# Performance work log

Hardware: AMD Instinct MI355X
Metric: run time of the kernel (lower is better)

Reference implementation:

```python
import jax, jax.numpy as jnp
import numpy as np


def setup_inputs() -> dict:
    key = jax.random.key(0)
    k1, k2, k3, k4 = jax.random.split(key, 4)
    N, T, F = 8192, 128, 9
    M_s = 256
    merged = jax.random.normal(k1, (N, T, F), dtype=jnp.float32)
    input1 = jax.random.normal(k2, (N, T, F), dtype=jnp.float32)
    samples = jax.random.normal(k3, (N, M_s), dtype=jnp.float32)
    labels = jax.random.randint(k4, (N,), 0, 10, dtype=jnp.int32)
    return {"merged": merged, "input1": input1, "samples": samples, "labels": labels}


def reference(merged, input1, samples, labels):
    # Pairwise squared distances S_ij = sum_k (s_i - s_j)^2 / M_s, computed via
    # the Gram-matrix identity instead of materializing the [N, N, M_s] tensor.
    M_s = samples.shape[1]
    sq = jnp.sum(samples * samples, axis=-1)                 # [N]
    gram = jnp.einsum('im,jm->ij', samples, samples)         # [N, N]
    S_ij = (sq[:, None] + sq[None, :] - 2.0 * gram) / jnp.float32(M_s)
    same = (labels[:, None] == labels[None, :]).astype(jnp.float32)
    term2 = jnp.mean(jnp.maximum(0.0, (1.0 - same) * (1.0 - S_ij)))
    L_label = 10.0 * jnp.mean(same * S_ij) + 10.0 * term2
    return L_label
```

## Files before the change

kernel.cpp:

```cpp
#include <hip/hip_runtime.h>

#define NROWS 8192
#define KDIM  256
#define NT    64
#define NBLK  (NT * (NT + 1) / 2)
#define GRID  256

typedef __attribute__((ext_vector_type(4)))  float f32x4;
typedef __attribute__((ext_vector_type(16))) float f32x16;
typedef __attribute__((ext_vector_type(4)))  int   i32x4;
typedef __attribute__((ext_vector_type(8)))  int   i32x8;

#define GLD(gp, lp)                                                            \
  __builtin_amdgcn_global_load_lds(                                            \
      (const __attribute__((address_space(1))) void*)(gp),                     \
      (__attribute__((address_space(3))) void*)(lp), 16, 0, 0)

__global__ void prep_kernel(const float* __restrict__ samples,
                            const int* __restrict__ labels,
                            unsigned char* __restrict__ sf8,
                            float2* __restrict__ meta,
                            float* __restrict__ out) {
  int row = blockIdx.x, t = threadIdx.x;
  float2 v2 = ((const float2*)samples)[(size_t)row * 128 + t];
  int pk = __builtin_amdgcn_cvt_pk_fp8_f32(v2.x, v2.y, 0, false);
  ((unsigned short*)sf8)[(size_t)row * 128 + t] = (unsigned short)(pk & 0xffff);
  float p = v2.x * v2.x + v2.y * v2.y;
#pragma unroll
  for (int off = 32; off; off >>= 1) p += __shfl_down(p, off);
  __shared__ float ws2[2];
  if ((t & 63) == 0) ws2[t >> 6] = p;
  __syncthreads();
  if (t == 0) {
    float tot = ws2[0] + ws2[1];
    meta[row] = make_float2(tot * (1.0f / 256.0f), (float)labels[row]);
  }
  if (row == 0 && t == 0) out[0] = 0.0f;
}

__device__ inline void decode_tile(int b, int& bi, int& bj) {
  float disc = (2.0f * NT + 1.0f) * (2.0f * NT + 1.0f) - 8.0f * (float)b;
  bi = (int)(((2.0f * NT + 1.0f) - sqrtf(disc)) * 0.5f);
  if (bi < 0) bi = 0;
  if (bi > NT - 1) bi = NT - 1;
  while (bi > 0 && (bi * NT - bi * (bi - 1) / 2) > b) --bi;
  while (((bi + 1) * NT - (bi + 1) * bi / 2) <= b) ++bi;
  bj = bi + (b - (bi * NT - bi * (bi - 1) / 2));
}

__global__ __launch_bounds__(512, 1) void pair_kernel(
    const unsigned char* __restrict__ sf8, const float2* __restrict__ meta,
    float* __restrict__ out) {

  __shared__ __align__(16) unsigned char As[2][128 * 256];
  __shared__ __align__(16) unsigned char Bs[2][128 * 256];
  __shared__ float red[8];

  int t = threadIdx.x;
  int lane = t & 63;
  int w = t >> 6;
  int wm = w >> 1, wn = w & 1;
  int lr = lane >> 4, pc = lane & 15;
  int l31 = lane & 31;
  int hk  = lane >> 5;

  float stt = 0.f;

  auto stage = [&](int bi_, int bj_, int buf) {
    int rA = bi_ * 128, rB = bj_ * 128;
#pragma unroll
    for (int p = 0; p < 4; ++p) {
      int region = p * 8 + w;
      int rr = region * 4 + lr;
      int c = pc ^ (rr & 15);
      GLD(sf8 + (size_t)(rA + rr) * KDIM + c * 16, &As[buf][region * 1024]);
      GLD(sf8 + (size_t)(rB + rr) * KDIM + c * 16, &Bs[buf][region * 1024]);
    }
  };

  int tile = blockIdx.x;
  int bi, bj;
  decode_tile(tile, bi, bj);
  stage(bi, bj, 0);
  int cur = 0;

  int pbi = 0, pbj = 0;
  float sqa[16], laa[16], sqb[2], labv[2], pwt = 1.f;
  f32x16 accA[2], accB[2];

  auto load_scalars = [&](int pbi_, int pbj_) {
#pragma unroll
    for (int g = 0; g < 4; ++g) {
      int gr = pbi_ * 128 + wm * 32 + g * 8 + 4 * hk;
      f32x4 m0 = *(const f32x4*)(meta + gr);
      f32x4 m1 = *(const f32x4*)(meta + gr + 2);
      sqa[g * 4 + 0] = m0.x; laa[g * 4 + 0] = m0.y;
      sqa[g * 4 + 1] = m0.z; laa[g * 4 + 1] = m0.w;
      sqa[g * 4 + 2] = m1.x; laa[g * 4 + 2] = m1.y;
      sqa[g * 4 + 3] = m1.z; laa[g * 4 + 3] = m1.w;
    }
#pragma unroll
    for (int j = 0; j < 2; ++j) {
      float2 mb = meta[pbj_ * 128 + wn * 64 + j * 32 + l31];
      sqb[j] = mb.x; labv[j] = mb.y;
    }
    pwt = (pbi_ == pbj_) ? 1.0f : 2.0f;
  };

  auto domfma = [&](f32x16 (&acc)[2]) {
#pragma unroll
    for (int j = 0; j < 2; ++j)
#pragma unroll
      for (int e = 0; e < 16; ++e) acc[j][e] = 0.f;
#pragma unroll
    for (int kt = 0; kt < 4; ++kt) {
      int c0 = kt * 4 + hk * 2;
      int m = wm * 32 + l31;
      const unsigned char* ab = &As[cur][m * 256];
      int sm = m & 15;
      i32x4 alo = *(const i32x4*)(ab + ((c0 ^ sm) << 4));
      i32x4 ahi = *(const i32x4*)(ab + (((c0 + 1) ^ sm) << 4));
      i32x8 av = {alo.x, alo.y, alo.z, alo.w, ahi.x, ahi.y, ahi.z, ahi.w};
#pragma unroll
      for (int j = 0; j < 2; ++j) {
        int n = wn * 64 + j * 32 + l31;
        const unsigned char* bb = &Bs[cur][n * 256];
        int sn = n & 15;
        i32x4 blo = *(const i32x4*)(bb + ((c0 ^ sn) << 4));
        i32x4 bhi = *(const i32x4*)(bb + (((c0 + 1) ^ sn) << 4));
        i32x8 bv = {blo.x, blo.y, blo.z, blo.w, bhi.x, bhi.y, bhi.z, bhi.w};
        acc[j] = __builtin_amdgcn_mfma_scale_f32_32x32x64_f8f6f4(
            av, bv, acc[j], 0, 0, 0, 127, 0, 127);
      }
    }
  };

  auto epi = [&](const f32x16 (&acc)[2]) {
    float s = 0.f;
#pragma unroll
    for (int j = 0; j < 2; ++j) {
#pragma unroll
      for (int g2 = 0; g2 < 16; ++g2) {
        float S = sqa[g2] + sqb[j] - acc[j][g2] * (1.0f / 128.0f);
        float h = fmaxf(0.f, 1.f - S);
        s += (laa[g2] == labv[j]) ? S : h;
      }
    }
    stt += pwt * s;
  };

  int k = 0;
  while (tile < NBLK) {
    int ntile = tile + GRID;
    int nbi = 0, nbj = 0;
    bool have_next = ntile < NBLK;
    if (have_next) decode_tile(ntile, nbi, nbj);

    __syncthreads();

    bool have_prev = (k > 0);
    if (have_prev) load_scalars(pbi, pbj);

    if (have_next) stage(nbi, nbj, cur ^ 1);

    if (k & 1) {
      domfma(accB);
      if (have_prev) epi(accA);
    } else {
      domfma(accA);
      if (have_prev) epi(accB);
    }

    pbi = bi; pbj = bj;
    tile = ntile; bi = nbi; bj = nbj; cur ^= 1; ++k;
  }

  load_scalars(pbi, pbj);
  if ((k - 1) & 1) epi(accB);
  else             epi(accA);

#pragma unroll
  for (int off = 32; off; off >>= 1) stt += __shfl_down(stt, off);
  if (lane == 0) red[w] = stt;
  __syncthreads();
  if (t == 0) {
    float a = 0.f;
#pragma unroll
    for (int q = 0; q < 8; q++) a += red[q];
    atomicAdd(&out[0], a * (10.0f / ((float)NROWS * (float)NROWS)));
  }
}

extern "C" void kernel_launch(void* const* d_in, const int* in_sizes, int n_in,
                              void* d_out, int out_size, void* d_ws,
                              size_t ws_size, hipStream_t stream) {
  const float* samples = (const float*)d_in[2];
  const int*   labels  = (const int*)d_in[3];

  char* ws = (char*)d_ws;
  unsigned char* sf8 = (unsigned char*)ws;
  float2* meta = (float2*)(ws + (size_t)NROWS * KDIM);
  float* out   = (float*)d_out;

  prep_kernel<<<NROWS, 128, 0, stream>>>(samples, labels, sf8, meta, out);
  pair_kernel<<<GRID, 512, 0, stream>>>(sf8, meta, out);
}
```

Before: 123.1 us.

## Assign contiguous tile ranges per block to reuse A tiles; widen prep kernel

```diff
diff --git a/kernel.cpp b/kernel.cpp
--- a/kernel.cpp
+++ b/kernel.cpp
@@ -16,26 +16,27 @@
       (const __attribute__((address_space(1))) void*)(gp),                     \
       (__attribute__((address_space(3))) void*)(lp), 16, 0, 0)
 
-__global__ void prep_kernel(const float* __restrict__ samples,
-                            const int* __restrict__ labels,
-                            unsigned char* __restrict__ sf8,
-                            float2* __restrict__ meta,
-                            float* __restrict__ out) {
-  int row = blockIdx.x, t = threadIdx.x;
-  float2 v2 = ((const float2*)samples)[(size_t)row * 128 + t];
-  int pk = __builtin_amdgcn_cvt_pk_fp8_f32(v2.x, v2.y, 0, false);
-  ((unsigned short*)sf8)[(size_t)row * 128 + t] = (unsigned short)(pk & 0xffff);
-  float p = v2.x * v2.x + v2.y * v2.y;
-#pragma unroll
-  for (int off = 32; off; off >>= 1) p += __shfl_down(p, off);
-  __shared__ float ws2[2];
-  if ((t & 63) == 0) ws2[t >> 6] = p;
-  __syncthreads();
-  if (t == 0) {
-    float tot = ws2[0] + ws2[1];
-    meta[row] = make_float2(tot * (1.0f / 256.0f), (float)labels[row]);
+__global__ __launch_bounds__(256) void prep_kernel(
+    const float* __restrict__ samples, const int* __restrict__ labels,
+    unsigned char* __restrict__ sf8, float2* __restrict__ meta,
+    float* __restrict__ out) {
+  int tid = blockIdx.x * 256 + threadIdx.x;
+  int gw = tid >> 6;
+  int lane = tid & 63;
+#pragma unroll
+  for (int it = 0; it < NROWS / 1024; ++it) {
+    int row = gw + it * 1024;
+    f32x4 v = ((const f32x4*)samples)[(size_t)row * 64 + lane];
+    int pk = __builtin_amdgcn_cvt_pk_fp8_f32(v.x, v.y, 0, false);
+    pk = __builtin_amdgcn_cvt_pk_fp8_f32(v.z, v.w, pk, true);
+    ((unsigned int*)sf8)[(size_t)row * 64 + lane] = (unsigned int)pk;
+    float p = v.x * v.x + v.y * v.y + v.z * v.z + v.w * v.w;
+#pragma unroll
+    for (int off = 32; off; off >>= 1) p += __shfl_down(p, off);
+    if (lane == 0)
+      meta[row] = make_float2(p * (1.0f / 256.0f), (float)labels[row]);
   }
-  if (row == 0 && t == 0) out[0] = 0.0f;
+  if (tid == 0) out[0] = 0.0f;
 }
 
 __device__ inline void decode_tile(int b, int& bi, int& bj) {
@@ -66,23 +67,36 @@
 
   float stt = 0.f;
 
-  auto stage = [&](int bi_, int bj_, int buf) {
-    int rA = bi_ * 128, rB = bj_ * 128;
+  auto stage_A = [&](int bi_, int buf) {
+    int rA = bi_ * 128;
 #pragma unroll
     for (int p = 0; p < 4; ++p) {
       int region = p * 8 + w;
       int rr = region * 4 + lr;
       int c = pc ^ (rr & 15);
       GLD(sf8 + (size_t)(rA + rr) * KDIM + c * 16, &As[buf][region * 1024]);
+    }
+  };
+  auto stage_B = [&](int bj_, int buf) {
+    int rB = bj_ * 128;
+#pragma unroll
+    for (int p = 0; p < 4; ++p) {
+      int region = p * 8 + w;
+      int rr = region * 4 + lr;
+      int c = pc ^ (rr & 15);
       GLD(sf8 + (size_t)(rB + rr) * KDIM + c * 16, &Bs[buf][region * 1024]);
     }
   };
 
-  int tile = blockIdx.x;
+  int cid = (blockIdx.x & 7) * 32 + (blockIdx.x >> 3);
+  int t0 = (cid * 65) >> 3, t1 = ((cid + 1) * 65) >> 3;
+  int ntile = t1 - t0;
+
   int bi, bj;
-  decode_tile(tile, bi, bj);
-  stage(bi, bj, 0);
-  int cur = 0;
+  decode_tile(t0, bi, bj);
+  stage_A(bi, 0);
+  stage_B(bj, 0);
+  int acur = 0, bcur = 0;
 
   int pbi = 0, pbj = 0;
   float sqa[16], laa[16], sqb[2], labv[2], pwt = 1.f;
@@ -112,11 +126,13 @@
     for (int j = 0; j < 2; ++j)
 #pragma unroll
       for (int e = 0; e < 16; ++e) acc[j][e] = 0.f;
+    const unsigned char* Ab = &As[acur][0];
+    const unsigned char* Bb = &Bs[bcur][0];
 #pragma unroll
     for (int kt = 0; kt < 4; ++kt) {
       int c0 = kt * 4 + hk * 2;
       int m = wm * 32 + l31;
-      const unsigned char* ab = &As[cur][m * 256];
+      const unsigned char* ab = Ab + m * 256;
       int sm = m & 15;
       i32x4 alo = *(const i32x4*)(ab + ((c0 ^ sm) << 4));
       i32x4 ahi = *(const i32x4*)(ab + (((c0 + 1) ^ sm) << 4));
@@ -124,7 +140,7 @@
 #pragma unroll
       for (int j = 0; j < 2; ++j) {
         int n = wn * 64 + j * 32 + l31;
-        const unsigned char* bb = &Bs[cur][n * 256];
+        const unsigned char* bb = Bb + n * 256;
         int sn = n & 15;
         i32x4 blo = *(const i32x4*)(bb + ((c0 ^ sn) << 4));
         i32x4 bhi = *(const i32x4*)(bb + (((c0 + 1) ^ sn) << 4));
@@ -149,35 +165,39 @@
     stt += pwt * s;
   };
 
-  int k = 0;
-  while (tile < NBLK) {
-    int ntile = tile + GRID;
-    int nbi = 0, nbj = 0;
-    bool have_next = ntile < NBLK;
-    if (have_next) decode_tile(ntile, nbi, nbj);
+  for (int k = 0; k < ntile; ++k) {
+    bool have_next = (k + 1 < ntile);
+    int nbi = bi, nbj = bj + 1;
+    if (nbj == NT) { nbi = bi + 1; nbj = nbi; }
 
     __syncthreads();
 
-    bool have_prev = (k > 0);
-    if (have_prev) load_scalars(pbi, pbj);
-
-    if (have_next) stage(nbi, nbj, cur ^ 1);
+    if (k > 0) load_scalars(pbi, pbj);
+
+    if (have_next) {
+      stage_B(nbj, bcur ^ 1);
+      if (nbi != bi) stage_A(nbi, acur ^ 1);
+    }
 
     if (k & 1) {
       domfma(accB);
-      if (have_prev) epi(accA);
+      if (k > 0) epi(accA);
     } else {
       domfma(accA);
-      if (have_prev) epi(accB);
+      if (k > 0) epi(accB);
     }
 
     pbi = bi; pbj = bj;
-    tile = ntile; bi = nbi; bj = nbj; cur ^= 1; ++k;
+    if (have_next) {
+      if (nbi != bi) acur ^= 1;
+      bcur ^= 1;
+      bi = nbi; bj = nbj;
+    }
   }
 
   load_scalars(pbi, pbj);
-  if ((k - 1) & 1) epi(accB);
-  else             epi(accA);
+  if ((ntile - 1) & 1) epi(accB);
+  else                 epi(accA);
 
 #pragma unroll
   for (int off = 32; off; off >>= 1) stt += __shfl_down(stt, off);
@@ -202,6 +222,6 @@
   float2* meta = (float2*)(ws + (size_t)NROWS * KDIM);
   float* out   = (float*)d_out;
 
-  prep_kernel<<<NROWS, 128, 0, stream>>>(samples, labels, sf8, meta, out);
+  prep_kernel<<<GRID, 256, 0, stream>>>(samples, labels, sf8, meta, out);
   pair_kernel<<<GRID, 512, 0, stream>>>(sf8, meta, out);
 }
```

Result: no change. 124.8 us (+1.4%).

## Fuse fp8 prep into pair kernel with a software grid barrier

Applied to the files above, without the earlier changes.

```diff
diff --git a/kernel.cpp b/kernel.cpp
--- a/kernel.cpp
+++ b/kernel.cpp
@@ -5,6 +5,7 @@
 #define NT    64
 #define NBLK  (NT * (NT + 1) / 2)
 #define GRID  256
+#define BARMAGIC 0xA5C3F00Du
 
 typedef __attribute__((ext_vector_type(4)))  float f32x4;
 typedef __attribute__((ext_vector_type(16))) float f32x16;
@@ -15,28 +16,6 @@
   __builtin_amdgcn_global_load_lds(                                            \
       (const __attribute__((address_space(1))) void*)(gp),                     \
       (__attribute__((address_space(3))) void*)(lp), 16, 0, 0)
-
-__global__ void prep_kernel(const float* __restrict__ samples,
-                            const int* __restrict__ labels,
-                            unsigned char* __restrict__ sf8,
-                            float2* __restrict__ meta,
-                            float* __restrict__ out) {
-  int row = blockIdx.x, t = threadIdx.x;
-  float2 v2 = ((const float2*)samples)[(size_t)row * 128 + t];
-  int pk = __builtin_amdgcn_cvt_pk_fp8_f32(v2.x, v2.y, 0, false);
-  ((unsigned short*)sf8)[(size_t)row * 128 + t] = (unsigned short)(pk & 0xffff);
-  float p = v2.x * v2.x + v2.y * v2.y;
-#pragma unroll
-  for (int off = 32; off; off >>= 1) p += __shfl_down(p, off);
-  __shared__ float ws2[2];
-  if ((t & 63) == 0) ws2[t >> 6] = p;
-  __syncthreads();
-  if (t == 0) {
-    float tot = ws2[0] + ws2[1];
-    meta[row] = make_float2(tot * (1.0f / 256.0f), (float)labels[row]);
-  }
-  if (row == 0 && t == 0) out[0] = 0.0f;
-}
 
 __device__ inline void decode_tile(int b, int& bi, int& bj) {
   float disc = (2.0f * NT + 1.0f) * (2.0f * NT + 1.0f) - 8.0f * (float)b;
@@ -48,9 +27,10 @@
   bj = bi + (b - (bi * NT - bi * (bi - 1) / 2));
 }
 
-__global__ __launch_bounds__(512, 1) void pair_kernel(
-    const unsigned char* __restrict__ sf8, const float2* __restrict__ meta,
-    float* __restrict__ out) {
+__global__ __launch_bounds__(512, 1) void fused_kernel(
+    const float* __restrict__ samples, const int* __restrict__ labels,
+    unsigned char* __restrict__ sf8, float2* __restrict__ meta,
+    unsigned int* __restrict__ bar, float* __restrict__ out) {
 
   __shared__ __align__(16) unsigned char As[2][128 * 256];
   __shared__ __align__(16) unsigned char Bs[2][128 * 256];
@@ -63,6 +43,40 @@
   int lr = lane >> 4, pc = lane & 15;
   int l31 = lane & 31;
   int hk  = lane >> 5;
+
+  {
+    int row0 = blockIdx.x * 32 + w * 4;
+#pragma unroll
+    for (int it = 0; it < 4; ++it) {
+      int row = row0 + it;
+      f32x4 v = ((const f32x4*)samples)[(size_t)row * 64 + lane];
+      int pk = __builtin_amdgcn_cvt_pk_fp8_f32(v.x, v.y, 0, false);
+      pk = __builtin_amdgcn_cvt_pk_fp8_f32(v.z, v.w, pk, true);
+      ((unsigned int*)sf8)[(size_t)row * 64 + lane] = (unsigned int)pk;
+      float p = v.x * v.x + v.y * v.y + v.z * v.z + v.w * v.w;
+#pragma unroll
+      for (int off = 32; off; off >>= 1) p += __shfl_down(p, off);
+      if (lane == 0)
+        meta[row] = make_float2(p * (1.0f / 256.0f), (float)labels[row]);
+    }
+    if (blockIdx.x == 0 && t == 0) out[0] = 0.0f;
+  }
+
+  __syncthreads();
+  if (t == 0) {
+    __threadfence();
+    __hip_atomic_store(&bar[blockIdx.x], BARMAGIC ^ (unsigned)blockIdx.x,
+                       __ATOMIC_RELAXED, __HIP_MEMORY_SCOPE_AGENT);
+  }
+  if (t < 256) {
+    unsigned int want = BARMAGIC ^ (unsigned)t;
+    while (__hip_atomic_load(&bar[t], __ATOMIC_RELAXED,
+                             __HIP_MEMORY_SCOPE_AGENT) != want) {
+    }
+  }
+  __syncthreads();
+  if (t == 0) __threadfence();
+  __syncthreads();
 
   float stt = 0.f;
 
@@ -200,8 +214,9 @@
   char* ws = (char*)d_ws;
   unsigned char* sf8 = (unsigned char*)ws;
   float2* meta = (float2*)(ws + (size_t)NROWS * KDIM);
-  float* out   = (float*)d_out;
-
-  prep_kernel<<<NROWS, 128, 0, stream>>>(samples, labels, sf8, meta, out);
-  pair_kernel<<<GRID, 512, 0, stream>>>(sf8, meta, out);
+  unsigned int* bar =
+      (unsigned int*)(ws + (size_t)NROWS * KDIM + NROWS * 8);
+  float* out = (float*)d_out;
+
+  fused_kernel<<<GRID, 512, 0, stream>>>(samples, labels, sf8, meta, bar, out);
 }
```

Result: slower. 136.8 us (+11.2%).

## Double pair-kernel waves to 16 per block and make prep kernel persistent

Applied to the files above, without the earlier changes.

```diff
diff --git a/kernel.cpp b/kernel.cpp
--- a/kernel.cpp
+++ b/kernel.cpp
@@ -16,26 +16,27 @@
       (const __attribute__((address_space(1))) void*)(gp),                     \
       (__attribute__((address_space(3))) void*)(lp), 16, 0, 0)
 
-__global__ void prep_kernel(const float* __restrict__ samples,
-                            const int* __restrict__ labels,
-                            unsigned char* __restrict__ sf8,
-                            float2* __restrict__ meta,
-                            float* __restrict__ out) {
-  int row = blockIdx.x, t = threadIdx.x;
-  float2 v2 = ((const float2*)samples)[(size_t)row * 128 + t];
-  int pk = __builtin_amdgcn_cvt_pk_fp8_f32(v2.x, v2.y, 0, false);
-  ((unsigned short*)sf8)[(size_t)row * 128 + t] = (unsigned short)(pk & 0xffff);
-  float p = v2.x * v2.x + v2.y * v2.y;
+__global__ __launch_bounds__(256) void prep_kernel(
+    const float* __restrict__ samples, const int* __restrict__ labels,
+    unsigned char* __restrict__ sf8, float2* __restrict__ meta,
+    float* __restrict__ out) {
+  int tid = blockIdx.x * 256 + threadIdx.x;
+  int gw = tid >> 6;
+  int lane = tid & 63;
 #pragma unroll
-  for (int off = 32; off; off >>= 1) p += __shfl_down(p, off);
-  __shared__ float ws2[2];
-  if ((t & 63) == 0) ws2[t >> 6] = p;
-  __syncthreads();
-  if (t == 0) {
-    float tot = ws2[0] + ws2[1];
-    meta[row] = make_float2(tot * (1.0f / 256.0f), (float)labels[row]);
+  for (int it = 0; it < NROWS / 1024; ++it) {
+    int row = gw + it * 1024;
+    f32x4 v = ((const f32x4*)samples)[(size_t)row * 64 + lane];
+    int pk = __builtin_amdgcn_cvt_pk_fp8_f32(v.x, v.y, 0, false);
+    pk = __builtin_amdgcn_cvt_pk_fp8_f32(v.z, v.w, pk, true);
+    ((unsigned int*)sf8)[(size_t)row * 64 + lane] = (unsigned int)pk;
+    float p = v.x * v.x + v.y * v.y + v.z * v.z + v.w * v.w;
+#pragma unroll
+    for (int off = 32; off; off >>= 1) p += __shfl_down(p, off);
+    if (lane == 0)
+      meta[row] = make_float2(p * (1.0f / 256.0f), (float)labels[row]);
   }
-  if (row == 0 && t == 0) out[0] = 0.0f;
+  if (tid == 0) out[0] = 0.0f;
 }
 
 __device__ inline void decode_tile(int b, int& bi, int& bj) {
@@ -48,18 +49,18 @@
   bj = bi + (b - (bi * NT - bi * (bi - 1) / 2));
 }
 
-__global__ __launch_bounds__(512, 1) void pair_kernel(
+__global__ __launch_bounds__(1024, 4) void pair_kernel(
     const unsigned char* __restrict__ sf8, const float2* __restrict__ meta,
     float* __restrict__ out) {
 
   __shared__ __align__(16) unsigned char As[2][128 * 256];
   __shared__ __align__(16) unsigned char Bs[2][128 * 256];
-  __shared__ float red[8];
+  __shared__ float red[16];
 
   int t = threadIdx.x;
   int lane = t & 63;
   int w = t >> 6;
-  int wm = w >> 1, wn = w & 1;
+  int wm = w >> 2, wn = w & 3;
   int lr = lane >> 4, pc = lane & 15;
   int l31 = lane & 31;
   int hk  = lane >> 5;
@@ -69,8 +70,8 @@
   auto stage = [&](int bi_, int bj_, int buf) {
     int rA = bi_ * 128, rB = bj_ * 128;
 #pragma unroll
-    for (int p = 0; p < 4; ++p) {
-      int region = p * 8 + w;
+    for (int p = 0; p < 2; ++p) {
+      int region = p * 16 + w;
       int rr = region * 4 + lr;
       int c = pc ^ (rr & 15);
       GLD(sf8 + (size_t)(rA + rr) * KDIM + c * 16, &As[buf][region * 1024]);
@@ -85,8 +86,8 @@
   int cur = 0;
 
   int pbi = 0, pbj = 0;
-  float sqa[16], laa[16], sqb[2], labv[2], pwt = 1.f;
-  f32x16 accA[2], accB[2];
+  float sqa[16], laa[16], sqbv = 0.f, labv = 0.f, pwt = 1.f;
+  f32x16 accA, accB;
 
   auto load_scalars = [&](int pbi_, int pbj_) {
 #pragma unroll
@@ -99,52 +100,39 @@
       sqa[g * 4 + 2] = m1.x; laa[g * 4 + 2] = m1.y;
       sqa[g * 4 + 3] = m1.z; laa[g * 4 + 3] = m1.w;
     }
-#pragma unroll
-    for (int j = 0; j < 2; ++j) {
-      float2 mb = meta[pbj_ * 128 + wn * 64 + j * 32 + l31];
-      sqb[j] = mb.x; labv[j] = mb.y;
-    }
+    float2 mb = meta[pbj_ * 128 + wn * 32 + l31];
+    sqbv = mb.x; labv = mb.y;
     pwt = (pbi_ == pbj_) ? 1.0f : 2.0f;
   };
 
-  auto domfma = [&](f32x16 (&acc)[2]) {
+  auto domfma = [&](f32x16& acc) {
 #pragma unroll
-    for (int j = 0; j < 2; ++j)
-#pragma unroll
-      for (int e = 0; e < 16; ++e) acc[j][e] = 0.f;
+    for (int e = 0; e < 16; ++e) acc[e] = 0.f;
+    int m = wm * 32 + l31, n = wn * 32 + l31;
+    const unsigned char* ab = &As[cur][m * 256];
+    const unsigned char* bb = &Bs[cur][n * 256];
+    int sm = m & 15, sn = n & 15;
 #pragma unroll
     for (int kt = 0; kt < 4; ++kt) {
       int c0 = kt * 4 + hk * 2;
-      int m = wm * 32 + l31;
-      const unsigned char* ab = &As[cur][m * 256];
-      int sm = m & 15;
       i32x4 alo = *(const i32x4*)(ab + ((c0 ^ sm) << 4));
       i32x4 ahi = *(const i32x4*)(ab + (((c0 + 1) ^ sm) << 4));
       i32x8 av = {alo.x, alo.y, alo.z, alo.w, ahi.x, ahi.y, ahi.z, ahi.w};
-#pragma unroll
-      for (int j = 0; j < 2; ++j) {
-        int n = wn * 64 + j * 32 + l31;
-        const unsigned char* bb = &Bs[cur][n * 256];
-        int sn = n & 15;
-        i32x4 blo = *(const i32x4*)(bb + ((c0 ^ sn) << 4));
-        i32x4 bhi = *(const i32x4*)(bb + (((c0 + 1) ^ sn) << 4));
-        i32x8 bv = {blo.x, blo.y, blo.z, blo.w, bhi.x, bhi.y, bhi.z, bhi.w};
-        acc[j] = __builtin_amdgcn_mfma_scale_f32_32x32x64_f8f6f4(
-            av, bv, acc[j], 0, 0, 0, 127, 0, 127);
-      }
+      i32x4 blo = *(const i32x4*)(bb + ((c0 ^ sn) << 4));
+      i32x4 bhi = *(const i32x4*)(bb + (((c0 + 1) ^ sn) << 4));
+      i32x8 bv = {blo.x, blo.y, blo.z, blo.w, bhi.x, bhi.y, bhi.z, bhi.w};
+      acc = __builtin_amdgcn_mfma_scale_f32_32x32x64_f8f6f4(
+          av, bv, acc, 0, 0, 0, 127, 0, 127);
     }
   };
 
-  auto epi = [&](const f32x16 (&acc)[2]) {
+  auto epi = [&](const f32x16& acc) {
     float s = 0.f;
 #pragma unroll
-    for (int j = 0; j < 2; ++j) {
-#pragma unroll
-      for (int g2 = 0; g2 < 16; ++g2) {
-        float S = sqa[g2] + sqb[j] - acc[j][g2] * (1.0f / 128.0f);
-        float h = fmaxf(0.f, 1.f - S);
-        s += (laa[g2] == labv[j]) ? S : h;
-      }
+    for (int g2 = 0; g2 < 16; ++g2) {
+      float S = sqa[g2] + sqbv - acc[g2] * (1.0f / 128.0f);
+      float h = fmaxf(0.f, 1.f - S);
+      s += (laa[g2] == labv) ? S : h;
     }
     stt += pwt * s;
   };
@@ -186,7 +174,7 @@
   if (t == 0) {
     float a = 0.f;
 #pragma unroll
-    for (int q = 0; q < 8; q++) a += red[q];
+    for (int q = 0; q < 16; q++) a += red[q];
     atomicAdd(&out[0], a * (10.0f / ((float)NROWS * (float)NROWS)));
   }
 }
@@ -202,6 +190,6 @@
   float2* meta = (float2*)(ws + (size_t)NROWS * KDIM);
   float* out   = (float*)d_out;
 
-  prep_kernel<<<NROWS, 128, 0, stream>>>(samples, labels, sf8, meta, out);
-  pair_kernel<<<GRID, 512, 0, stream>>>(sf8, meta, out);
+  prep_kernel<<<GRID, 256, 0, stream>>>(samples, labels, sf8, meta, out);
+  pair_kernel<<<GRID, 1024, 0, stream>>>(sf8, meta, out);
 }
```

Result: slower. 229.4 us (+86.4%).
